# Optimization experiments

Measured on AMD Instinct MI355X. Metric: run time of the kernel, lower is better.

## Reference

```python
import jax, jax.numpy as jnp
import numpy as np
from jax.ops import segment_sum

N_NODES = 100000


def _gcn_norm(src, dst, n):
    # add self-loops, compute symmetric normalization deg^-1/2 * deg^-1/2
    loop = jnp.arange(n, dtype=src.dtype)
    src_sl = jnp.concatenate([src, loop])
    dst_sl = jnp.concatenate([dst, loop])
    deg = segment_sum(jnp.ones_like(src_sl, dtype=jnp.float32), dst_sl, num_segments=n)
    dinv = jnp.where(deg > 0, jax.lax.rsqrt(deg), 0.0)
    norm = dinv[src_sl] * dinv[dst_sl]  # [E+N]
    return src_sl, dst_sl, norm


def _gcn_conv(x, W, b, src_sl, dst_sl, norm, n):
    h = x @ W                              # [N, out]  dense GEMM first (smaller msg dim)
    msg = h[src_sl] * norm[:, None]        # [E+N, out]
    out = segment_sum(msg, dst_sl, num_segments=n)
    return out + b


def setup_inputs() -> dict:
    key = jax.random.key(0)
    k1, k2, k3, k4, k5 = jax.random.split(key, 5)
    x = jax.random.normal(k1, (N_NODES, 400), dtype=jnp.float32)
    edge_index = jax.random.randint(k2, (2, 3200000), 0, N_NODES, dtype=jnp.int64)
    batch = jnp.zeros((N_NODES,), dtype=jnp.int64)
    # Glorot-style init like PyG GCNConv
    W1 = jax.random.normal(k3, (400, 128), dtype=jnp.float32) * (1.0 / np.sqrt(400))
    b1 = jnp.zeros((128,), dtype=jnp.float32)
    W2 = jax.random.normal(k4, (128, 128), dtype=jnp.float32) * (1.0 / np.sqrt(128))
    b2 = jnp.zeros((128,), dtype=jnp.float32)
    return {"x": x, "edge_index": edge_index, "batch": batch,
            "W1": W1, "b1": b1, "W2": W2, "b2": b2}


def reference(x, edge_index, batch, W1, b1, W2, b2):
    n = x.shape[0]
    src, dst = edge_index[0], edge_index[1]
    src_sl, dst_sl, norm = _gcn_norm(src, dst, n)
    h = jax.nn.relu(_gcn_conv(x, W1, b1, src_sl, dst_sl, norm, n))
    h = jax.nn.relu(_gcn_conv(h, W2, b2, src_sl, dst_sl, norm, n))
    return h
```

## Files before the change

kernel.cpp:

```cpp
#include <hip/hip_runtime.h>


#define NBMAX 1024
#define HB    128
#define CAPB  4608

using u16 = unsigned short;
using u32 = unsigned int;
typedef __attribute__((ext_vector_type(8))) short short8;
typedef __attribute__((ext_vector_type(4))) float f32x4;

__device__ __forceinline__ u16 f2bf(float f) {
    u32 u = __float_as_uint(f);
    u += 0x7fffu + ((u >> 16) & 1u);
    return (u16)(u >> 16);
}
__device__ __forceinline__ u32 pack2(float a, float b) {
    return (u32)f2bf(a) | ((u32)f2bf(b) << 16);
}
__device__ __forceinline__ float bflo(u32 u) { return __uint_as_float(u << 16); }
__device__ __forceinline__ float bfhi(u32 u) { return __uint_as_float(u & 0xffff0000u); }


__global__ __launch_bounds__(256) void k_init_bcur(u32* bcur, int NB) {
    int b = blockIdx.x * 256 + threadIdx.x;
    if (b < NB) bcur[b] = (u32)b * CAPB;
}

__global__ __launch_bounds__(256) void k_scatter(const int* __restrict__ src,
                                                 const int* __restrict__ dst,
                                                 u32* __restrict__ bcur,
                                                 u32* __restrict__ ebuf,
                                                 int E, int NB) {
    __shared__ u32 hist[NBMAX];
    __shared__ u32 base[NBMAX];
    const int tid = threadIdx.x;
    for (int i = tid; i < NB; i += 256) hist[i] = 0u;
    __syncthreads();
    const int chunk = (E + gridDim.x - 1) / gridDim.x;
    const int e0 = blockIdx.x * chunk;
    const int e1 = min(E, e0 + chunk);
    for (int i = e0 + tid; i < e1; i += 256)
        atomicAdd(&hist[dst[i] >> 7], 1u);
    __syncthreads();
    for (int i = tid; i < NB; i += 256) {
        const u32 c = hist[i];
        base[i] = c ? atomicAdd(&bcur[i], c) : 0u;
    }
    __syncthreads();
    for (int i = tid; i < NB; i += 256) hist[i] = 0u;
    __syncthreads();
    for (int i = e0 + tid; i < e1; i += 256) {
        const int s = src[i];
        const int d = dst[i];
        const int b = d >> 7;
        const u32 loc = atomicAdd(&hist[b], 1u);
        ebuf[base[b] + loc] = ((u32)(d & 127) << 17) | (u32)s;
    }
}

__global__ __launch_bounds__(256) void k_csr_build(const u32* __restrict__ ebuf,
                                                   const u32* __restrict__ bcur,
                                                   int* __restrict__ rowbeg,
                                                   u16* __restrict__ deg16,
                                                   float* __restrict__ dinv,
                                                   int* __restrict__ csr_s,
                                                   int N, int NB) {
    __shared__ u32 cnt128[128];
    __shared__ u32 scan128[128];
    __shared__ u32 cur128[128];
    const int tid = threadIdx.x;
    const int b = blockIdx.x;
    const int r0 = b * CAPB;
    const int r1 = (int)bcur[b];

    if (tid < 128) cnt128[tid] = 0u;
    __syncthreads();
    for (int i = r0 + tid; i < r1; i += 256)
        atomicAdd(&cnt128[ebuf[i] >> 17], 1u);
    __syncthreads();

    if (tid < 128) scan128[tid] = cnt128[tid];
    __syncthreads();
    for (int off = 1; off < 128; off <<= 1) {
        u32 v = 0;
        if (tid < 128) {
            v = scan128[tid];
            if (tid >= off) v += scan128[tid - off];
        }
        __syncthreads();
        if (tid < 128) scan128[tid] = v;
        __syncthreads();
    }

    if (tid < 128) {
        const u32 dg   = cnt128[tid];
        const u32 excl = scan128[tid] - dg;
        cur128[tid] = excl;
        const int node = b * 128 + tid;
        if (node < N) {
            rowbeg[node] = r0 + (int)excl;
            deg16[node]  = (u16)dg;
            dinv[node]   = rsqrtf((float)(dg + 1u));
        }
    }
    __syncthreads();

    for (int i = r0 + tid; i < r1; i += 256) {
        const u32 e = ebuf[i];
        const u32 p = atomicAdd(&cur128[e >> 17], 1u);
        csr_s[r0 + (int)p] = (int)(e & 0x1FFFFu);
    }
}

__global__ __launch_bounds__(256) void k_wprep(const float* __restrict__ W,
                                               u16* __restrict__ Wt,
                                               int K, int KP) {
    int idx = blockIdx.x * 256 + threadIdx.x;
    if (idx >= 128 * KP) return;
    int n = idx / KP, k = idx - n * KP;
    Wt[idx] = (k < K) ? f2bf(W[(size_t)k * 128 + n]) : (u16)0;
}

template <int ABF>
__global__ __launch_bounds__(512) void k_gemm_mfma(
        const void* __restrict__ Aptr,
        const u16* __restrict__ Wt,
        const float* __restrict__ dinv,
        u16* __restrict__ H, int M, int K, int KP) {
    __shared__ u16 smem[16384];
    u16* As = smem;
    u16* Bs = smem + 128 * 64;

    const int tid = threadIdx.x;
    const int row0 = blockIdx.x * 128;
    const int wid = tid >> 6;
    const int lane = tid & 63;
    const int wm = wid >> 2, wn = wid & 3;
    const int l15 = lane & 15, lg = lane >> 4;
    const int lr7 = l15 & 7;

    const int arow = tid >> 2;
    const int achk = tid & 3;
    const int grow = row0 + arow;
    const int ar7 = arow & 7;
    const int s0 = (achk * 2) ^ ar7;
    const int s1 = (achk * 2 + 1) ^ ar7;

    float4 ar0, ar1, ar2, ar3;
    uint4  au0, au1;
    uint4  bu0, bu1;

    auto load_tile = [&](int kt) {
        const int k0 = kt * 64 + achk * 16;
        if (ABF) {
            if (grow < M) {
                const u16* ap = (const u16*)Aptr + (size_t)grow * K + k0;
                au0 = *reinterpret_cast<const uint4*>(ap);
                au1 = *reinterpret_cast<const uint4*>(ap + 8);
            } else {
                au0 = make_uint4(0, 0, 0, 0);
                au1 = make_uint4(0, 0, 0, 0);
            }
        } else {
            if (grow < M && k0 < K) {
                const float* ap = (const float*)Aptr + (size_t)grow * K + k0;
                ar0 = *reinterpret_cast<const float4*>(ap);
                ar1 = *reinterpret_cast<const float4*>(ap + 4);
                ar2 = *reinterpret_cast<const float4*>(ap + 8);
                ar3 = *reinterpret_cast<const float4*>(ap + 12);
            } else {
                ar0 = ar1 = ar2 = ar3 = make_float4(0.f, 0.f, 0.f, 0.f);
            }
        }
        const u16* wp = Wt + (size_t)arow * KP + k0;
        bu0 = *reinterpret_cast<const uint4*>(wp);
        bu1 = *reinterpret_cast<const uint4*>(wp + 8);
    };

    auto store_tile = [&]() {
        uint4 w0, w1;
        if (ABF) {
            w0 = au0; w1 = au1;
        } else {
            w0.x = pack2(ar0.x, ar0.y); w0.y = pack2(ar0.z, ar0.w);
            w0.z = pack2(ar1.x, ar1.y); w0.w = pack2(ar1.z, ar1.w);
            w1.x = pack2(ar2.x, ar2.y); w1.y = pack2(ar2.z, ar2.w);
            w1.z = pack2(ar3.x, ar3.y); w1.w = pack2(ar3.z, ar3.w);
        }
        u16* ad = As + arow * 64;
        *reinterpret_cast<uint4*>(ad + s0 * 8) = w0;
        *reinterpret_cast<uint4*>(ad + s1 * 8) = w1;
        u16* bd = Bs + arow * 64;
        *reinterpret_cast<uint4*>(bd + s0 * 8) = bu0;
        *reinterpret_cast<uint4*>(bd + s1 * 8) = bu1;
    };

    f32x4 acc[4][2];
#pragma unroll
    for (int i = 0; i < 4; ++i)
#pragma unroll
        for (int j = 0; j < 2; ++j)
            acc[i][j] = (f32x4){0.f, 0.f, 0.f, 0.f};

    const int NT = KP >> 6;
    load_tile(0);
    for (int kt = 0; kt < NT; ++kt) {
        __syncthreads();
        store_tile();
        __syncthreads();
        if (kt + 1 < NT) load_tile(kt + 1);
#pragma unroll
        for (int sub = 0; sub < 2; ++sub) {
            const int slot = ((sub * 4 + lg) ^ lr7) * 8;
            short8 af[4], bf[2];
#pragma unroll
            for (int i = 0; i < 4; ++i)
                af[i] = *reinterpret_cast<const short8*>(
                    As + (wm * 64 + i * 16 + l15) * 64 + slot);
#pragma unroll
            for (int j = 0; j < 2; ++j)
                bf[j] = *reinterpret_cast<const short8*>(
                    Bs + (wn * 32 + j * 16 + l15) * 64 + slot);
#pragma unroll
            for (int i = 0; i < 4; ++i)
#pragma unroll
                for (int j = 0; j < 2; ++j)
                    acc[i][j] = __builtin_amdgcn_mfma_f32_16x16x32_bf16(
                        af[i], bf[j], acc[i][j], 0, 0, 0);
        }
    }

    const int CSTR = 136;
    __syncthreads();
#pragma unroll
    for (int half = 0; half < 2; ++half) {
        if (wm == half) {
#pragma unroll
            for (int i = 0; i < 4; ++i)
#pragma unroll
                for (int r = 0; r < 4; ++r) {
                    const int gr = row0 + half * 64 + i * 16 + lg * 4 + r;
                    const float dv = (gr < M) ? dinv[gr] : 0.f;
#pragma unroll
                    for (int j = 0; j < 2; ++j)
                        smem[(i * 16 + lg * 4 + r) * CSTR + wn * 32 + j * 16 + l15] =
                            f2bf(acc[i][j][r] * dv);
                }
        }
        __syncthreads();
        {
            const int rr = tid >> 3;
            const int cc = (tid & 7) * 16;
            const int gr = row0 + half * 64 + rr;
            if (gr < M) {
                const u16* cp = smem + rr * CSTR + cc;
                uint4 q0 = *reinterpret_cast<const uint4*>(cp);
                uint4 q1 = *reinterpret_cast<const uint4*>(cp + 8);
                uint4* hp = reinterpret_cast<uint4*>(H + (size_t)gr * 128 + cc);
                hp[0] = q0; hp[1] = q1;
            }
        }
        __syncthreads();
    }
}

template <int OUTBF>
__global__ __launch_bounds__(256) void k_gather(const int* __restrict__ rowbeg,
                                                const u16* __restrict__ deg16,
                                                const float* __restrict__ dinv,
                                                const int* __restrict__ csr_s,
                                                const u16* __restrict__ H,
                                                const float* __restrict__ bias,
                                                void* __restrict__ outp, int N) {
    const int t = threadIdx.x;
    const int node = blockIdx.x * 16 + (t >> 4);
    if (node >= N) return;
    const int lane = t & 15;
    const int c8 = lane * 8;

    const uint4 hv = *reinterpret_cast<const uint4*>(H + (size_t)node * 128 + c8);
    float acc0 = bflo(hv.x), acc1 = bfhi(hv.x);
    float acc2 = bflo(hv.y), acc3 = bfhi(hv.y);
    float acc4 = bflo(hv.z), acc5 = bfhi(hv.z);
    float acc6 = bflo(hv.w), acc7 = bfhi(hv.w);

    const int beg = rowbeg[node];
    const int end = beg + (int)deg16[node];
    for (int r = beg; r < end; r += 16) {
        const int cntc = min(16, end - r);
        int sv = (lane < cntc) ? csr_s[r + lane] : 0;
        for (int j = 0; j < cntc; ++j) {
            const int s = __shfl(sv, j, 16);
            const uint4 x = *reinterpret_cast<const uint4*>(H + (size_t)s * 128 + c8);
            acc0 += bflo(x.x); acc1 += bfhi(x.x);
            acc2 += bflo(x.y); acc3 += bfhi(x.y);
            acc4 += bflo(x.z); acc5 += bfhi(x.z);
            acc6 += bflo(x.w); acc7 += bfhi(x.w);
        }
    }

    const float dv = dinv[node];
    const float4 b0 = *reinterpret_cast<const float4*>(bias + c8);
    const float4 b1 = *reinterpret_cast<const float4*>(bias + c8 + 4);
    const float r0 = fmaxf(fmaf(acc0, dv, b0.x), 0.f);
    const float r1 = fmaxf(fmaf(acc1, dv, b0.y), 0.f);
    const float r2 = fmaxf(fmaf(acc2, dv, b0.z), 0.f);
    const float r3 = fmaxf(fmaf(acc3, dv, b0.w), 0.f);
    const float r4 = fmaxf(fmaf(acc4, dv, b1.x), 0.f);
    const float r5 = fmaxf(fmaf(acc5, dv, b1.y), 0.f);
    const float r6 = fmaxf(fmaf(acc6, dv, b1.z), 0.f);
    const float r7 = fmaxf(fmaf(acc7, dv, b1.w), 0.f);

    if (OUTBF) {
        uint4 q;
        q.x = pack2(r0, r1); q.y = pack2(r2, r3);
        q.z = pack2(r4, r5); q.w = pack2(r6, r7);
        u16* op = (u16*)outp + (size_t)node * 128 + c8;
        *reinterpret_cast<uint4*>(op) = q;
    } else {
        float* op = (float*)outp + (size_t)node * 128 + c8;
        *reinterpret_cast<float4*>(op)     = make_float4(r0, r1, r2, r3);
        *reinterpret_cast<float4*>(op + 4) = make_float4(r4, r5, r6, r7);
    }
}


extern "C" void kernel_launch(void* const* d_in, const int* in_sizes, int n_in,
                              void* d_out, int out_size, void* d_ws, size_t ws_size,
                              hipStream_t stream) {
    const float* x  = (const float*)d_in[0];
    const int*   ei = (const int*)d_in[1];
    const float* W1 = (const float*)d_in[3];
    const float* b1 = (const float*)d_in[4];
    const float* W2 = (const float*)d_in[5];
    const float* b2 = (const float*)d_in[6];
    float* out = (float*)d_out;

    const int N = in_sizes[0] / 400;
    const int E = in_sizes[1] / 2;
    const int* src = ei;
    const int* dst = ei + E;
    const int NB = (N + 127) >> 7;
    const int KP1 = 448;
    const int KP2 = 128;

    char* ws = (char*)d_ws;
    size_t off = 0;
    auto alloc = [&](size_t bytes) {
        void* p = ws + off;
        off = (off + bytes + 255) & ~(size_t)255;
        return p;
    };
    u32*   bcur   = (u32*)alloc((size_t)NB * 4);
    int*   rowbeg = (int*)alloc((size_t)N * 4);
    u16*   deg16  = (u16*)alloc((size_t)N * 2);
    float* dinv   = (float*)alloc((size_t)N * 4);
    int*   csr_s  = (int*)alloc((size_t)NB * CAPB * 4);
    u32*   ebuf   = (u32*)alloc((size_t)NB * CAPB * 4);
    u16*   hs     = (u16*)alloc((size_t)N * 128 * 2);
    u16*   abf    = (u16*)alloc((size_t)N * 128 * 2);
    u16*   Wt1    = (u16*)alloc((size_t)128 * KP1 * 2);
    u16*   Wt2    = (u16*)alloc((size_t)128 * KP2 * 2);

    const int nb_gm = (N + 127) / 128;
    const int nb_g  = (N + 15) / 16;

    k_wprep<<<(128 * KP1 + 255) / 256, 256, 0, stream>>>(W1, Wt1, 400, KP1);
    k_wprep<<<(128 * KP2 + 255) / 256, 256, 0, stream>>>(W2, Wt2, 128, KP2);

    k_init_bcur<<<(NB + 255) / 256, 256, 0, stream>>>(bcur, NB);
    k_scatter<<<HB, 256, 0, stream>>>(src, dst, bcur, ebuf, E, NB);
    k_csr_build<<<NB, 256, 0, stream>>>(ebuf, bcur, rowbeg, deg16, dinv, csr_s, N, NB);

    k_gemm_mfma<0><<<nb_gm, 512, 0, stream>>>(x, Wt1, dinv, hs, N, 400, KP1);
    k_gather<1><<<nb_g, 256, 0, stream>>>(rowbeg, deg16, dinv, csr_s, hs, b1, abf, N);

    k_gemm_mfma<1><<<nb_gm, 512, 0, stream>>>(abf, Wt2, dinv, hs, N, 128, KP2);
    k_gather<0><<<nb_g, 256, 0, stream>>>(rowbeg, deg16, dinv, csr_s, hs, b2, out, N);
}
```

Baseline: 439.7 us.

## Sort CSR neighbors by source tile and sweep gather in source-tile phases

CSR build now buckets each destination's edges by source tile (src>>13), so neighbor lists are sorted by coarse source region. The gather kernel processes four nodes per 16-lane group and walks source tiles in lockstep, synchronizing the block between tiles. The aim is for concurrently running blocks to touch a limited window of H at a time and improve L2 locality for the random row gathers. The cost is larger LDS use and scan work in csr_build, extra ballot and loop overhead, and block-wide barriers per tile, which only loosely align accesses across blocks.

```diff
diff --git a/kernel.cpp b/kernel.cpp
--- a/kernel.cpp
+++ b/kernel.cpp
@@ -4,6 +4,7 @@
 #define NBMAX 1024
 #define HB    128
 #define CAPB  4608
+#define TSLOG 13
 
 using u16 = unsigned short;
 using u32 = unsigned int;
@@ -66,40 +67,54 @@
                                                    float* __restrict__ dinv,
                                                    int* __restrict__ csr_s,
                                                    int N, int NB) {
-    __shared__ u32 cnt128[128];
-    __shared__ u32 scan128[128];
-    __shared__ u32 cur128[128];
+    __shared__ u32 cnt[2048];
+    __shared__ u32 scan[2048];
+    __shared__ u32 cur[2048];
+    __shared__ u32 bsum[256];
     const int tid = threadIdx.x;
     const int b = blockIdx.x;
     const int r0 = b * CAPB;
     const int r1 = (int)bcur[b];
 
-    if (tid < 128) cnt128[tid] = 0u;
-    __syncthreads();
-    for (int i = r0 + tid; i < r1; i += 256)
-        atomicAdd(&cnt128[ebuf[i] >> 17], 1u);
-    __syncthreads();
-
-    if (tid < 128) scan128[tid] = cnt128[tid];
-    __syncthreads();
-    for (int off = 1; off < 128; off <<= 1) {
-        u32 v = 0;
-        if (tid < 128) {
-            v = scan128[tid];
-            if (tid >= off) v += scan128[tid - off];
-        }
-        __syncthreads();
-        if (tid < 128) scan128[tid] = v;
-        __syncthreads();
-    }
+    for (int i = tid; i < 2048; i += 256) cnt[i] = 0u;
+    __syncthreads();
+    for (int i = r0 + tid; i < r1; i += 256) {
+        const u32 e = ebuf[i];
+        const u32 key = ((e >> 17) << 4) | ((e & 0x1FFFFu) >> TSLOG);
+        atomicAdd(&cnt[key], 1u);
+    }
+    __syncthreads();
+
+    const int i8 = tid * 8;
+    u32 pre[8];
+    u32 run = 0;
+#pragma unroll
+    for (int j = 0; j < 8; ++j) { pre[j] = run; run += cnt[i8 + j]; }
+    bsum[tid] = run;
+    __syncthreads();
+    for (int off = 1; off < 256; off <<= 1) {
+        u32 v = bsum[tid];
+        u32 add = (tid >= off) ? bsum[tid - off] : 0u;
+        __syncthreads();
+        bsum[tid] = v + add;
+        __syncthreads();
+    }
+    const u32 excl = bsum[tid] - run;
+#pragma unroll
+    for (int j = 0; j < 8; ++j) {
+        const u32 x = excl + pre[j];
+        scan[i8 + j] = x;
+        cur[i8 + j] = x;
+    }
+    __syncthreads();
 
     if (tid < 128) {
-        const u32 dg   = cnt128[tid];
-        const u32 excl = scan128[tid] - dg;
-        cur128[tid] = excl;
+        const u32 beg  = scan[tid * 16];
+        const u32 endv = (tid == 127) ? (u32)(r1 - r0) : scan[(tid + 1) * 16];
+        const u32 dg   = endv - beg;
         const int node = b * 128 + tid;
         if (node < N) {
-            rowbeg[node] = r0 + (int)excl;
+            rowbeg[node] = r0 + (int)beg;
             deg16[node]  = (u16)dg;
             dinv[node]   = rsqrtf((float)(dg + 1u));
         }
@@ -108,8 +123,10 @@
 
     for (int i = r0 + tid; i < r1; i += 256) {
         const u32 e = ebuf[i];
-        const u32 p = atomicAdd(&cur128[e >> 17], 1u);
-        csr_s[r0 + (int)p] = (int)(e & 0x1FFFFu);
+        const u32 sr = e & 0x1FFFFu;
+        const u32 key = ((e >> 17) << 4) | (sr >> TSLOG);
+        const u32 p = atomicAdd(&cur[key], 1u);
+        csr_s[r0 + (int)p] = (int)sr;
     }
 }
 
@@ -266,62 +283,92 @@
 }
 
 template <int OUTBF>
-__global__ __launch_bounds__(256) void k_gather(const int* __restrict__ rowbeg,
-                                                const u16* __restrict__ deg16,
-                                                const float* __restrict__ dinv,
-                                                const int* __restrict__ csr_s,
-                                                const u16* __restrict__ H,
-                                                const float* __restrict__ bias,
-                                                void* __restrict__ outp, int N) {
+__global__ __launch_bounds__(256, 6) void k_gather(const int* __restrict__ rowbeg,
+                                                   const u16* __restrict__ deg16,
+                                                   const float* __restrict__ dinv,
+                                                   const int* __restrict__ csr_s,
+                                                   const u16* __restrict__ H,
+                                                   const float* __restrict__ bias,
+                                                   void* __restrict__ outp,
+                                                   int N, int NT) {
     const int t = threadIdx.x;
-    const int node = blockIdx.x * 16 + (t >> 4);
-    if (node >= N) return;
     const int lane = t & 15;
     const int c8 = lane * 8;
-
-    const uint4 hv = *reinterpret_cast<const uint4*>(H + (size_t)node * 128 + c8);
-    float acc0 = bflo(hv.x), acc1 = bfhi(hv.x);
-    float acc2 = bflo(hv.y), acc3 = bfhi(hv.y);
-    float acc4 = bflo(hv.z), acc5 = bfhi(hv.z);
-    float acc6 = bflo(hv.w), acc7 = bfhi(hv.w);
-
-    const int beg = rowbeg[node];
-    const int end = beg + (int)deg16[node];
-    for (int r = beg; r < end; r += 16) {
-        const int cntc = min(16, end - r);
-        int sv = (lane < cntc) ? csr_s[r + lane] : 0;
-        for (int j = 0; j < cntc; ++j) {
-            const int s = __shfl(sv, j, 16);
-            const uint4 x = *reinterpret_cast<const uint4*>(H + (size_t)s * 128 + c8);
-            acc0 += bflo(x.x); acc1 += bfhi(x.x);
-            acc2 += bflo(x.y); acc3 += bfhi(x.y);
-            acc4 += bflo(x.z); acc5 += bfhi(x.z);
-            acc6 += bflo(x.w); acc7 += bfhi(x.w);
-        }
-    }
-
-    const float dv = dinv[node];
+    const int gw = (t & 63) >> 4;
+    const int n0 = blockIdx.x * 64 + (t >> 4);
+
+    float acc[4][8];
+    int rr[4], re[4];
+#pragma unroll
+    for (int s = 0; s < 4; ++s) {
+        const int node = n0 + s * 16;
+        rr[s] = 0; re[s] = 0;
+#pragma unroll
+        for (int j = 0; j < 8; ++j) acc[s][j] = 0.f;
+        if (node < N) {
+            const uint4 hv = *reinterpret_cast<const uint4*>(H + (size_t)node * 128 + c8);
+            acc[s][0] = bflo(hv.x); acc[s][1] = bfhi(hv.x);
+            acc[s][2] = bflo(hv.y); acc[s][3] = bfhi(hv.y);
+            acc[s][4] = bflo(hv.z); acc[s][5] = bfhi(hv.z);
+            acc[s][6] = bflo(hv.w); acc[s][7] = bfhi(hv.w);
+            rr[s] = rowbeg[node];
+            re[s] = rr[s] + (int)deg16[node];
+        }
+    }
+
+    for (int tt = 0; tt < NT; ++tt) {
+        const int bound = (tt + 1 >= NT) ? 0x7FFFFFFF : ((tt + 1) << TSLOG);
+#pragma unroll
+        for (int s = 0; s < 4; ++s) {
+            int r = rr[s];
+            const int end = re[s];
+            while (r < end) {
+                const int cnt = min(16, end - r);
+                const int sv = (lane < cnt) ? csr_s[r + lane] : 0x7FFFFFFF;
+                const unsigned long long m = __ballot(sv < bound);
+                const int take = __popc((u32)((m >> (gw * 16)) & 0xFFFFull));
+                for (int j = 0; j < take; ++j) {
+                    const int sn = __shfl(sv, j, 16);
+                    const uint4 x = *reinterpret_cast<const uint4*>(H + (size_t)sn * 128 + c8);
+                    acc[s][0] += bflo(x.x); acc[s][1] += bfhi(x.x);
+                    acc[s][2] += bflo(x.y); acc[s][3] += bfhi(x.y);
+                    acc[s][4] += bflo(x.z); acc[s][5] += bfhi(x.z);
+                    acc[s][6] += bflo(x.w); acc[s][7] += bfhi(x.w);
+                }
+                r += take;
+                if (take < cnt) break;
+            }
+            rr[s] = r;
+        }
+        __syncthreads();
+    }
+
     const float4 b0 = *reinterpret_cast<const float4*>(bias + c8);
     const float4 b1 = *reinterpret_cast<const float4*>(bias + c8 + 4);
-    const float r0 = fmaxf(fmaf(acc0, dv, b0.x), 0.f);
-    const float r1 = fmaxf(fmaf(acc1, dv, b0.y), 0.f);
-    const float r2 = fmaxf(fmaf(acc2, dv, b0.z), 0.f);
-    const float r3 = fmaxf(fmaf(acc3, dv, b0.w), 0.f);
-    const float r4 = fmaxf(fmaf(acc4, dv, b1.x), 0.f);
-    const float r5 = fmaxf(fmaf(acc5, dv, b1.y), 0.f);
-    const float r6 = fmaxf(fmaf(acc6, dv, b1.z), 0.f);
-    const float r7 = fmaxf(fmaf(acc7, dv, b1.w), 0.f);
-
-    if (OUTBF) {
-        uint4 q;
-        q.x = pack2(r0, r1); q.y = pack2(r2, r3);
-        q.z = pack2(r4, r5); q.w = pack2(r6, r7);
-        u16* op = (u16*)outp + (size_t)node * 128 + c8;
-        *reinterpret_cast<uint4*>(op) = q;
-    } else {
-        float* op = (float*)outp + (size_t)node * 128 + c8;
-        *reinterpret_cast<float4*>(op)     = make_float4(r0, r1, r2, r3);
-        *reinterpret_cast<float4*>(op + 4) = make_float4(r4, r5, r6, r7);
+#pragma unroll
+    for (int s = 0; s < 4; ++s) {
+        const int node = n0 + s * 16;
+        if (node >= N) continue;
+        const float dv = dinv[node];
+        const float r0 = fmaxf(fmaf(acc[s][0], dv, b0.x), 0.f);
+        const float r1 = fmaxf(fmaf(acc[s][1], dv, b0.y), 0.f);
+        const float r2 = fmaxf(fmaf(acc[s][2], dv, b0.z), 0.f);
+        const float r3 = fmaxf(fmaf(acc[s][3], dv, b0.w), 0.f);
+        const float r4 = fmaxf(fmaf(acc[s][4], dv, b1.x), 0.f);
+        const float r5 = fmaxf(fmaf(acc[s][5], dv, b1.y), 0.f);
+        const float r6 = fmaxf(fmaf(acc[s][6], dv, b1.z), 0.f);
+        const float r7 = fmaxf(fmaf(acc[s][7], dv, b1.w), 0.f);
+        if (OUTBF) {
+            uint4 q;
+            q.x = pack2(r0, r1); q.y = pack2(r2, r3);
+            q.z = pack2(r4, r5); q.w = pack2(r6, r7);
+            u16* op = (u16*)outp + (size_t)node * 128 + c8;
+            *reinterpret_cast<uint4*>(op) = q;
+        } else {
+            float* op = (float*)outp + (size_t)node * 128 + c8;
+            *reinterpret_cast<float4*>(op)     = make_float4(r0, r1, r2, r3);
+            *reinterpret_cast<float4*>(op + 4) = make_float4(r4, r5, r6, r7);
+        }
     }
 }
 
@@ -342,6 +389,7 @@
     const int* src = ei;
     const int* dst = ei + E;
     const int NB = (N + 127) >> 7;
+    const int NT = (N + (1 << TSLOG) - 1) >> TSLOG;
     const int KP1 = 448;
     const int KP2 = 128;
 
@@ -364,7 +412,7 @@
     u16*   Wt2    = (u16*)alloc((size_t)128 * KP2 * 2);
 
     const int nb_gm = (N + 127) / 128;
-    const int nb_g  = (N + 15) / 16;
+    const int nb_g  = (N + 63) / 64;
 
     k_wprep<<<(128 * KP1 + 255) / 256, 256, 0, stream>>>(W1, Wt1, 400, KP1);
     k_wprep<<<(128 * KP2 + 255) / 256, 256, 0, stream>>>(W2, Wt2, 128, KP2);
@@ -374,8 +422,8 @@
     k_csr_build<<<NB, 256, 0, stream>>>(ebuf, bcur, rowbeg, deg16, dinv, csr_s, N, NB);
 
     k_gemm_mfma<0><<<nb_gm, 512, 0, stream>>>(x, Wt1, dinv, hs, N, 400, KP1);
-    k_gather<1><<<nb_g, 256, 0, stream>>>(rowbeg, deg16, dinv, csr_s, hs, b1, abf, N);
+    k_gather<1><<<nb_g, 256, 0, stream>>>(rowbeg, deg16, dinv, csr_s, hs, b1, abf, N, NT);
 
     k_gemm_mfma<1><<<nb_gm, 512, 0, stream>>>(abf, Wt2, dinv, hs, N, 128, KP2);
-    k_gather<0><<<nb_g, 256, 0, stream>>>(rowbeg, deg16, dinv, csr_s, hs, b2, out, N);
-}
+    k_gather<0><<<nb_g, 256, 0, stream>>>(rowbeg, deg16, dinv, csr_s, hs, b2, out, N, NT);
+}
```

Measured after the change: 472.2 us. 7.4% more time.
